# Kernel tuning notes

Measured on AMD Instinct MI355X. Metric: run time of the kernel, lower is better.

The kernel has to match this reference:

```python
import jax, jax.numpy as jnp
import numpy as np

B, LQ, LM, D, H = 2, 2048, 2048, 1024, 16
DH = D // H  # 64

def setup_inputs() -> dict:
    key = jax.random.key(0)
    ks = jax.random.split(key, 11)
    s = 0.02
    return {
        "query": jax.random.normal(ks[0], (B, LQ, D), jnp.float32),
        "memory": jax.random.normal(ks[1], (B, LM, D), jnp.float32),
        "memory_bias": jax.random.normal(ks[2], (B, LM), jnp.float32),
        "Wq": jax.random.normal(ks[3], (D, D), jnp.float32) * s,
        "bq": jnp.zeros((D,), jnp.float32),
        "Wk": jax.random.normal(ks[4], (D, D), jnp.float32) * s,
        "bk": jnp.zeros((D,), jnp.float32),
        "Wv": jax.random.normal(ks[5], (D, D), jnp.float32) * s,
        "bv": jnp.zeros((D,), jnp.float32),
        "Wo": jax.random.normal(ks[6], (D, D), jnp.float32) * s,
        "bo": jnp.zeros((D,), jnp.float32),
    }

def reference(query, memory, memory_bias, Wq, bq, Wk, bk, Wv, bv, Wo, bo):
    # QKV projections, split into heads: [B, L, H, DH]
    q = (query @ Wq + bq).reshape(B, LQ, H, DH)
    k = (memory @ Wk + bk).reshape(B, LM, H, DH)
    v = (memory @ Wv + bv).reshape(B, LM, H, DH)
    q = q * (DH ** -0.5)
    # logits: [B, H, Lq, Lk] (matches torch.einsum('btnh,bfnh->bnft', k, q))
    logits = jnp.einsum("bfnh,btnh->bnft", q, k)
    logits = logits + memory_bias[:, None, None, :]  # bias [B, Lm] -> [B,1,1,Lk]
    weights = jax.nn.softmax(logits, axis=-1)
    # dropout omitted (eval / rate 0 for correctness baseline)
    attn = jnp.einsum("bnft,btnh->bfnh", weights, v).reshape(B, LQ, D)
    return attn @ Wo + bo  # [B, Lq, output_depth]
```

## Files before the change

### kernel.cpp

```cpp
#include <hip/hip_runtime.h>
#include <hip/hip_bf16.h>
#include <math.h>


typedef __bf16 bf16;
typedef __bf16 bf16x4 __attribute__((ext_vector_type(4)));
typedef __bf16 bf16x8 __attribute__((ext_vector_type(8)));
typedef float f32x4 __attribute__((ext_vector_type(4)));

#define MFMA16(a, b, c) __builtin_amdgcn_mfma_f32_16x16x32_bf16((a), (b), (c), 0, 0, 0)

__device__ inline float exp2_hw(float x) {
    float r; asm("v_exp_f32 %0, %1" : "=v"(r) : "v"(x)); return r;
}

__device__ inline void gload_lds16(const bf16* g, bf16* l) {
    __builtin_amdgcn_global_load_lds(
        (const __attribute__((address_space(1))) void*)g,
        (__attribute__((address_space(3))) void*)l, 16, 0, 0);
}

__global__ __launch_bounds__(256) void prep_kernel(
    const float* __restrict__ query, const float* __restrict__ memory,
    const float* __restrict__ mbias,
    const float* __restrict__ W0, const float* __restrict__ W1,
    const float* __restrict__ W2, const float* __restrict__ W3,
    bf16* __restrict__ Yq, bf16* __restrict__ Ym, float* __restrict__ sbias,
    bf16* __restrict__ T0, bf16* __restrict__ T1,
    bf16* __restrict__ T2, bf16* __restrict__ T3)
{
    __shared__ float Ls[64][65];
    const int t = threadIdx.x;

    if (blockIdx.z == 0) {
        const float* X = blockIdx.y ? memory : query;
        bf16* Y = blockIdx.y ? Ym : Yq;
        const size_t i = ((size_t)blockIdx.x * 256 + t) * 8;
        float4 f0 = *(const float4*)&X[i];
        float4 f1 = *(const float4*)&X[i + 4];
        bf16x8 h;
        h[0] = (bf16)f0.x; h[1] = (bf16)f0.y; h[2] = (bf16)f0.z; h[3] = (bf16)f0.w;
        h[4] = (bf16)f1.x; h[5] = (bf16)f1.y; h[6] = (bf16)f1.z; h[7] = (bf16)f1.w;
        *(bf16x8*)&Y[i] = h;
        return;
    }
    const int x = blockIdx.x;
    if (x == 1024) {
        const int i = blockIdx.y * 2048 + t * 8;
        #pragma unroll
        for (int j = 0; j < 8; ++j) sbias[i + j] = mbias[i + j] * 1.44269504f;
        return;
    }
    if (x > 1024 || blockIdx.y) return;

    const int wsel = x >> 8, sub = x & 255;
    const float* W; bf16* T;
    switch (wsel) {
        case 0:  W = W0; T = T0; break;
        case 1:  W = W1; T = T1; break;
        case 2:  W = W2; T = T2; break;
        default: W = W3; T = T3; break;
    }
    const int n0 = (sub & 15) * 64, k0 = (sub >> 4) * 64;
    const int g = t >> 4, c = (t & 15) * 4;
    #pragma unroll
    for (int p = 0; p < 4; ++p) {
        const int row = p * 16 + g;
        float4 f = *(const float4*)&W[(size_t)(k0 + row) * 1024 + n0 + c];
        Ls[row][c + 0] = f.x; Ls[row][c + 1] = f.y;
        Ls[row][c + 2] = f.z; Ls[row][c + 3] = f.w;
    }
    __syncthreads();
    #pragma unroll
    for (int p = 0; p < 4; ++p) {
        const int n = p * 16 + g;
        bf16x4 h;
        h[0] = (bf16)Ls[c + 0][n]; h[1] = (bf16)Ls[c + 1][n];
        h[2] = (bf16)Ls[c + 2][n]; h[3] = (bf16)Ls[c + 3][n];
        *(bf16x4*)&T[(size_t)(n0 + n) * 1024 + k0 + c] = h;
    }
}

template <typename TO>
__global__ __launch_bounds__(256) void gemm_kernel(
    const bf16* __restrict__ A, const bf16* __restrict__ WT,
    const float* __restrict__ bias, TO* __restrict__ out,
    float alpha, int mode)
{
    __shared__ __align__(16) bf16 As[2][128 * 64];
    __shared__ __align__(16) bf16 Bs[2][64 * 64];

    const int fid = blockIdx.x + (blockIdx.y << 4);
    const int swz = (fid & 7) * 64 + (fid >> 3);
    const int n0 = (swz & 15) * 64;
    const int m0 = (swz >> 4) * 128;

    const int tid = threadIdx.x;
    const int w = tid >> 6, lane = tid & 63;
    const int lr = lane & 15, lg = lane >> 4;
    const int wm = (w >> 1) * 64, wn = (w & 1) * 32;

    const int arow0 = w * 32 + (lane >> 3);
    const int brow0 = w * 16 + (lane >> 3);
    const int sch = lane & 7;

    f32x4 acc[4][2] = {};

    auto stageG = [&](int kt, int bi) {
        #pragma unroll
        for (int p = 0; p < 4; ++p) {
            const int row = arow0 + p * 8;
            const int xc = ((sch ^ (row & 7)) << 3);
            gload_lds16(&A[(size_t)(m0 + row) * 1024 + kt + xc],
                        &As[bi][row * 64 + sch * 8]);
        }
        #pragma unroll
        for (int p = 0; p < 2; ++p) {
            const int row = brow0 + p * 8;
            const int xc = ((sch ^ (row & 7)) << 3);
            gload_lds16(&WT[(size_t)(n0 + row) * 1024 + kt + xc],
                        &Bs[bi][row * 64 + sch * 8]);
        }
    };

    stageG(0, 0);
    __syncthreads();

    int cur = 0;
    #pragma unroll 1
    for (int t = 0; t < 16; ++t) {
        if (t < 15) stageG((t + 1) * 64, cur ^ 1);

        #pragma unroll
        for (int ks = 0; ks < 2; ++ks) {
            const int c = (((ks * 4 + lg) ^ (lr & 7)) << 3);
            bf16x8 af[4], bfv[2];
            #pragma unroll
            for (int mt = 0; mt < 4; ++mt)
                af[mt] = *(const bf16x8*)&As[cur][(wm + mt * 16 + lr) * 64 + c];
            #pragma unroll
            for (int nt = 0; nt < 2; ++nt)
                bfv[nt] = *(const bf16x8*)&Bs[cur][(wn + nt * 16 + lr) * 64 + c];
            #pragma unroll
            for (int nt = 0; nt < 2; ++nt)
                #pragma unroll
                for (int mt = 0; mt < 4; ++mt)
                    acc[mt][nt] = MFMA16(af[mt], bfv[nt], acc[mt][nt]);
        }
        __syncthreads();
        cur ^= 1;
    }

    #pragma unroll
    for (int nt = 0; nt < 2; ++nt) {
        const int n = n0 + wn + nt * 16 + lr;
        const float bv = bias[n];
        #pragma unroll
        for (int mt = 0; mt < 4; ++mt) {
            #pragma unroll
            for (int i = 0; i < 4; ++i) {
                const int m = m0 + wm + mt * 16 + lg * 4 + i;
                const float v = (acc[mt][nt][i] + bv) * alpha;
                if (mode == 0) {
                    out[(size_t)m * 1024 + n] = (TO)v;
                } else {
                    const int b = m >> 11, t2 = m & 2047;
                    out[((size_t)(b << 10) + n) * 2048 + t2] = (TO)v;
                }
            }
        }
    }
}

__global__ __launch_bounds__(256) void gemm_kv_kernel(
    const bf16* __restrict__ A, const bf16* __restrict__ WTk,
    const bf16* __restrict__ WTv, const float* __restrict__ bk,
    const float* __restrict__ bv, bf16* __restrict__ Kout,
    bf16* __restrict__ Vtout)
{
    __shared__ __align__(16) bf16 As[2][128 * 64];
    __shared__ __align__(16) bf16 Bk[2][64 * 64];
    __shared__ __align__(16) bf16 Bv[2][64 * 64];

    const int fid = blockIdx.x + (blockIdx.y << 4);
    const int swz = (fid & 7) * 64 + (fid >> 3);
    const int n0 = (swz & 15) * 64;
    const int m0 = (swz >> 4) * 128;

    const int tid = threadIdx.x;
    const int w = tid >> 6, lane = tid & 63;
    const int lr = lane & 15, lg = lane >> 4;
    const int wm = (w >> 1) * 64, wn = (w & 1) * 32;

    const int arow0 = w * 32 + (lane >> 3);
    const int brow0 = w * 16 + (lane >> 3);
    const int sch = lane & 7;

    f32x4 accK[4][2] = {}, accV[4][2] = {};

    auto stageG = [&](int kt, int bi) {
        #pragma unroll
        for (int p = 0; p < 4; ++p) {
            const int row = arow0 + p * 8;
            const int xc = ((sch ^ (row & 7)) << 3);
            gload_lds16(&A[(size_t)(m0 + row) * 1024 + kt + xc],
                        &As[bi][row * 64 + sch * 8]);
        }
        #pragma unroll
        for (int p = 0; p < 2; ++p) {
            const int row = brow0 + p * 8;
            const int xc = ((sch ^ (row & 7)) << 3);
            gload_lds16(&WTk[(size_t)(n0 + row) * 1024 + kt + xc],
                        &Bk[bi][row * 64 + sch * 8]);
            gload_lds16(&WTv[(size_t)(n0 + row) * 1024 + kt + xc],
                        &Bv[bi][row * 64 + sch * 8]);
        }
    };

    stageG(0, 0);
    __syncthreads();

    int cur = 0;
    #pragma unroll 1
    for (int t = 0; t < 16; ++t) {
        if (t < 15) stageG((t + 1) * 64, cur ^ 1);

        #pragma unroll
        for (int ks = 0; ks < 2; ++ks) {
            const int c = (((ks * 4 + lg) ^ (lr & 7)) << 3);
            bf16x8 af[4], bkf[2], bvf[2];
            #pragma unroll
            for (int mt = 0; mt < 4; ++mt)
                af[mt] = *(const bf16x8*)&As[cur][(wm + mt * 16 + lr) * 64 + c];
            #pragma unroll
            for (int nt = 0; nt < 2; ++nt) {
                bkf[nt] = *(const bf16x8*)&Bk[cur][(wn + nt * 16 + lr) * 64 + c];
                bvf[nt] = *(const bf16x8*)&Bv[cur][(wn + nt * 16 + lr) * 64 + c];
            }
            #pragma unroll
            for (int nt = 0; nt < 2; ++nt)
                #pragma unroll
                for (int mt = 0; mt < 4; ++mt) {
                    accK[mt][nt] = MFMA16(af[mt], bkf[nt], accK[mt][nt]);
                    accV[mt][nt] = MFMA16(af[mt], bvf[nt], accV[mt][nt]);
                }
        }
        __syncthreads();
        cur ^= 1;
    }

    #pragma unroll
    for (int nt = 0; nt < 2; ++nt) {
        const int n = n0 + wn + nt * 16 + lr;
        const float bkv = bk[n], bvv = bv[n];
        #pragma unroll
        for (int mt = 0; mt < 4; ++mt) {
            #pragma unroll
            for (int i = 0; i < 4; ++i) {
                const int m = m0 + wm + mt * 16 + lg * 4 + i;
                Kout[(size_t)m * 1024 + n] = (bf16)(accK[mt][nt][i] + bkv);
                const int b = m >> 11, t2 = m & 2047;
                Vtout[((size_t)(b << 10) + n) * 2048 + t2] = (bf16)(accV[mt][nt][i] + bvv);
            }
        }
    }
}

__global__ __launch_bounds__(256) void attn_kernel(
    const bf16* __restrict__ Q, const bf16* __restrict__ K,
    const bf16* __restrict__ Vt, const float* __restrict__ sbias,
    bf16* __restrict__ Oout)
{
    __shared__ __align__(16) bf16 Kbuf[4][4096];
    __shared__ __align__(16) bf16 Vbuf[4][4096];

    const int tid = threadIdx.x;
    const int w = tid >> 6, lane = tid & 63;
    const int lr = lane & 15, lg = lane >> 4;

    const int fid = blockIdx.x + (blockIdx.y << 4) + (blockIdx.z << 8);
    const int swz = (fid & 7) * 64 + (fid >> 3);
    const int qt = swz & 15, head = (swz >> 4) & 15, b = swz >> 8;
    const int qrow = qt * 128 + w * 32;

    bf16x8 qf[2][2];
    #pragma unroll
    for (int g = 0; g < 2; ++g) {
        const size_t qo = (size_t)(b * 2048 + qrow + g * 16 + lr) * 1024 + head * 64;
        qf[g][0] = *(const bf16x8*)&Q[qo + lg * 8];
        qf[g][1] = *(const bf16x8*)&Q[qo + 32 + lg * 8];
    }

    const bf16* Kb = K + (size_t)b * 2048 * 1024 + head * 64;
    const bf16* Vb = Vt + ((size_t)b * 1024 + head * 64) * 2048;
    const float* biasb = sbias + b * 2048;

    float m_run[2] = {-INFINITY, -INFINITY};
    f32x4 of[2][4] = {};
    f32x4 ofl[2] = {};

    bf16x8 ones8;
    #pragma unroll
    for (int j = 0; j < 8; ++j) ones8[j] = (bf16)1.0f;

    auto stage = [&](int t, int slot) {
        #pragma unroll
        for (int cp = 0; cp < 2; ++cp) {
            const int chunk = cp * 256 + tid;
            const int R = chunk >> 3, cc = chunk & 7;
            const int cs = cc ^ (R & 7);
            const int piR = ((R & 16) << 1) | ((R & 12) << 1) | ((R & 32) >> 3) | (R & 3);
            gload_lds16(Kb + (size_t)(t * 64 + piR) * 1024 + cs * 8,
                        &Kbuf[slot][chunk * 8]);
            gload_lds16(Vb + (size_t)R * 2048 + t * 64 + cs * 8,
                        &Vbuf[slot][chunk * 8]);
        }
    };

    stage(0, 0);
    stage(1, 1);

    #pragma unroll 1
    for (int it = 0; it < 32; ++it) {
        const int slot = it & 3;
        const int tn = (it < 30) ? it + 2 : 31;
        stage(tn, (it + 2) & 3);
        asm volatile("s_waitcnt vmcnt(8)" ::: "memory");
        __builtin_amdgcn_s_barrier();
        __builtin_amdgcn_sched_barrier(0);

        const int bt = it * 64;
        f32x4 b4[4];
        b4[0] = *(const f32x4*)&biasb[bt + 8 * lg];
        b4[1] = *(const f32x4*)&biasb[bt + 32 + 8 * lg];
        b4[2] = *(const f32x4*)&biasb[bt + 4 + 8 * lg];
        b4[3] = *(const f32x4*)&biasb[bt + 36 + 8 * lg];

        f32x4 s[2][4];
        #pragma unroll
        for (int g = 0; g < 2; ++g)
            #pragma unroll
            for (int nt = 0; nt < 4; ++nt) s[g][nt] = b4[nt];
        #pragma unroll
        for (int ks = 0; ks < 2; ++ks) {
            const int cw = (((ks * 4 + lg) ^ (lr & 7)) << 3);
            bf16x8 kf[4];
            #pragma unroll
            for (int nt = 0; nt < 4; ++nt)
                kf[nt] = *(const bf16x8*)&Kbuf[slot][(nt * 16 + lr) * 64 + cw];
            __builtin_amdgcn_s_setprio(1);
            #pragma unroll
            for (int nt = 0; nt < 4; ++nt) {
                s[0][nt] = MFMA16(kf[nt], qf[0][ks], s[0][nt]);
                s[1][nt] = MFMA16(kf[nt], qf[1][ks], s[1][nt]);
            }
            __builtin_amdgcn_s_setprio(0);
        }

        float rml[2];
        #pragma unroll
        for (int g = 0; g < 2; ++g) {
            float m0 = fmaxf(fmaxf(s[g][0][0], s[g][0][1]), fmaxf(s[g][0][2], s[g][0][3]));
            float m1 = fmaxf(fmaxf(s[g][1][0], s[g][1][1]), fmaxf(s[g][1][2], s[g][1][3]));
            float m2 = fmaxf(fmaxf(s[g][2][0], s[g][2][1]), fmaxf(s[g][2][2], s[g][2][3]));
            float m3 = fmaxf(fmaxf(s[g][3][0], s[g][3][1]), fmaxf(s[g][3][2], s[g][3][3]));
            rml[g] = fmaxf(fmaxf(m0, m1), fmaxf(m2, m3));
        }
        const bool need = (rml[0] > m_run[0] + 8.f) || (rml[1] > m_run[1] + 8.f);

        if (__any(need)) {
            #pragma unroll
            for (int g = 0; g < 2; ++g) {
                float mx = fmaxf(rml[g], __shfl_xor(rml[g], 16, 64));
                mx = fmaxf(mx, __shfl_xor(mx, 32, 64));
                const float mnew = fmaxf(m_run[g], mx);
                const float al = exp2_hw(m_run[g] - mnew);
                m_run[g] = mnew;
                ofl[g] *= al;
                #pragma unroll
                for (int dt = 0; dt < 4; ++dt) of[g][dt] *= al;
            }
        }

        bf16x8 pb[2][2];
        #pragma unroll
        for (int g = 0; g < 2; ++g)
            #pragma unroll
            for (int i = 0; i < 4; ++i) {
                pb[g][0][i]     = (bf16)exp2_hw(s[g][0][i] - m_run[g]);
                pb[g][1][i]     = (bf16)exp2_hw(s[g][1][i] - m_run[g]);
                pb[g][0][4 + i] = (bf16)exp2_hw(s[g][2][i] - m_run[g]);
                pb[g][1][4 + i] = (bf16)exp2_hw(s[g][3][i] - m_run[g]);
            }

        __builtin_amdgcn_s_setprio(1);
        #pragma unroll
        for (int ks = 0; ks < 2; ++ks) {
            const int cw = (((ks * 4 + lg) ^ (lr & 7)) << 3);
            bf16x8 vf[4];
            #pragma unroll
            for (int dt = 0; dt < 4; ++dt)
                vf[dt] = *(const bf16x8*)&Vbuf[slot][(dt * 16 + lr) * 64 + cw];
            #pragma unroll
            for (int g = 0; g < 2; ++g) {
                #pragma unroll
                for (int dt = 0; dt < 4; ++dt)
                    of[g][dt] = MFMA16(vf[dt], pb[g][ks], of[g][dt]);
                ofl[g] = MFMA16(ones8, pb[g][ks], ofl[g]);
            }
        }
        __builtin_amdgcn_s_setprio(0);
    }

    #pragma unroll
    for (int g = 0; g < 2; ++g) {
        const float inv = 1.0f / ofl[g][0];
        const size_t ob = (size_t)(b * 2048 + qrow + g * 16 + lr) * 1024 + head * 64;
        #pragma unroll
        for (int dt = 0; dt < 4; ++dt) {
            bf16x4 h4;
            #pragma unroll
            for (int i = 0; i < 4; ++i) h4[i] = (bf16)(of[g][dt][i] * inv);
            *(bf16x4*)&Oout[ob + dt * 16 + lg * 4] = h4;
        }
    }
}

extern "C" void kernel_launch(void* const* d_in, const int* in_sizes, int n_in,
                              void* d_out, int out_size, void* d_ws, size_t ws_size,
                              hipStream_t stream) {
    const float* query  = (const float*)d_in[0];
    const float* memory = (const float*)d_in[1];
    const float* mbias  = (const float*)d_in[2];
    const float* Wq = (const float*)d_in[3];
    const float* bq = (const float*)d_in[4];
    const float* Wk = (const float*)d_in[5];
    const float* bk = (const float*)d_in[6];
    const float* Wv = (const float*)d_in[7];
    const float* bv = (const float*)d_in[8];
    const float* Wo = (const float*)d_in[9];
    const float* bo = (const float*)d_in[10];
    float* out = (float*)d_out;

    const size_t SZ = 4096ull * 1024ull * sizeof(bf16);
    const size_t WZ = 1024ull * 1024ull * sizeof(bf16);
    char* ws = (char*)d_ws;
    bf16* Qp  = (bf16*)(ws);
    bf16* Kp  = (bf16*)(ws + SZ);
    bf16* Vtp = (bf16*)(ws + 2 * SZ);
    bf16* Ap  = (bf16*)(ws + 3 * SZ);
    bf16* WTq = (bf16*)(ws + 4 * SZ);
    bf16* WTk = (bf16*)(ws + 4 * SZ + WZ);
    bf16* WTv = (bf16*)(ws + 4 * SZ + 2 * WZ);
    bf16* WTo = (bf16*)(ws + 4 * SZ + 3 * WZ);
    float* sbias = (float*)(ws + 4 * SZ + 4 * WZ);

    dim3 blk(256);
    prep_kernel<<<dim3(2048, 2, 2), blk, 0, stream>>>(
        query, memory, mbias, Wq, Wk, Wv, Wo, Kp, Ap, sbias, WTq, WTk, WTv, WTo);

    dim3 gg(16, 32);
    gemm_kernel<bf16><<<gg, blk, 0, stream>>>(Kp, WTq, bq, Qp, 0.18033688f, 0);
    gemm_kv_kernel<<<gg, blk, 0, stream>>>(Ap, WTk, WTv, bk, bv, Kp, Vtp);
    attn_kernel<<<dim3(16, 16, 2), blk, 0, stream>>>(Qp, Kp, Vtp, sbias, Ap);
    gemm_kernel<float><<<gg, blk, 0, stream>>>(Ap, WTo, bo, out, 1.0f, 0);
}
```

Measured before the change: 129.3 us.

## Use 512-thread attention blocks sharing K/V tiles, prefetch bias and V fragments

```diff
diff --git a/kernel.cpp b/kernel.cpp
--- a/kernel.cpp
+++ b/kernel.cpp
@@ -266,7 +266,7 @@
     }
 }
 
-__global__ __launch_bounds__(256) void attn_kernel(
+__global__ __launch_bounds__(512) void attn_kernel(
     const bf16* __restrict__ Q, const bf16* __restrict__ K,
     const bf16* __restrict__ Vt, const float* __restrict__ sbias,
     bf16* __restrict__ Oout)
@@ -278,10 +278,10 @@
     const int w = tid >> 6, lane = tid & 63;
     const int lr = lane & 15, lg = lane >> 4;
 
-    const int fid = blockIdx.x + (blockIdx.y << 4) + (blockIdx.z << 8);
-    const int swz = (fid & 7) * 64 + (fid >> 3);
-    const int qt = swz & 15, head = (swz >> 4) & 15, b = swz >> 8;
-    const int qrow = qt * 128 + w * 32;
+    const int fid = blockIdx.x + (blockIdx.y << 3) + (blockIdx.z << 7);
+    const int swz = (fid & 7) * 32 + (fid >> 3);
+    const int qt = swz & 7, head = (swz >> 3) & 15, b = swz >> 7;
+    const int qrow = qt * 256 + w * 32;
 
     bf16x8 qf[2][2];
     #pragma unroll
@@ -303,38 +303,40 @@
     #pragma unroll
     for (int j = 0; j < 8; ++j) ones8[j] = (bf16)1.0f;
 
+    const int R = tid >> 3, cc = tid & 7;
+    const int cs = cc ^ (R & 7);
+    const int piR = ((R & 16) << 1) | ((R & 12) << 1) | ((R & 32) >> 3) | (R & 3);
     auto stage = [&](int t, int slot) {
-        #pragma unroll
-        for (int cp = 0; cp < 2; ++cp) {
-            const int chunk = cp * 256 + tid;
-            const int R = chunk >> 3, cc = chunk & 7;
-            const int cs = cc ^ (R & 7);
-            const int piR = ((R & 16) << 1) | ((R & 12) << 1) | ((R & 32) >> 3) | (R & 3);
-            gload_lds16(Kb + (size_t)(t * 64 + piR) * 1024 + cs * 8,
-                        &Kbuf[slot][chunk * 8]);
-            gload_lds16(Vb + (size_t)R * 2048 + t * 64 + cs * 8,
-                        &Vbuf[slot][chunk * 8]);
-        }
+        gload_lds16(Kb + (size_t)(t * 64 + piR) * 1024 + cs * 8,
+                    &Kbuf[slot][tid * 8]);
+        gload_lds16(Vb + (size_t)R * 2048 + t * 64 + cs * 8,
+                    &Vbuf[slot][tid * 8]);
     };
 
     stage(0, 0);
     stage(1, 1);
+
+    f32x4 b4[4];
+    b4[0] = *(const f32x4*)&biasb[8 * lg];
+    b4[1] = *(const f32x4*)&biasb[32 + 8 * lg];
+    b4[2] = *(const f32x4*)&biasb[4 + 8 * lg];
+    b4[3] = *(const f32x4*)&biasb[36 + 8 * lg];
 
     #pragma unroll 1
     for (int it = 0; it < 32; ++it) {
         const int slot = it & 3;
         const int tn = (it < 30) ? it + 2 : 31;
         stage(tn, (it + 2) & 3);
-        asm volatile("s_waitcnt vmcnt(8)" ::: "memory");
+        asm volatile("s_waitcnt vmcnt(4)" ::: "memory");
         __builtin_amdgcn_s_barrier();
         __builtin_amdgcn_sched_barrier(0);
 
-        const int bt = it * 64;
-        f32x4 b4[4];
-        b4[0] = *(const f32x4*)&biasb[bt + 8 * lg];
-        b4[1] = *(const f32x4*)&biasb[bt + 32 + 8 * lg];
-        b4[2] = *(const f32x4*)&biasb[bt + 4 + 8 * lg];
-        b4[3] = *(const f32x4*)&biasb[bt + 36 + 8 * lg];
+        const int bt = ((it < 31) ? it + 1 : 31) * 64;
+        f32x4 b4n[4];
+        b4n[0] = *(const f32x4*)&biasb[bt + 8 * lg];
+        b4n[1] = *(const f32x4*)&biasb[bt + 32 + 8 * lg];
+        b4n[2] = *(const f32x4*)&biasb[bt + 4 + 8 * lg];
+        b4n[3] = *(const f32x4*)&biasb[bt + 36 + 8 * lg];
 
         f32x4 s[2][4];
         #pragma unroll
@@ -355,6 +357,15 @@
                 s[1][nt] = MFMA16(kf[nt], qf[1][ks], s[1][nt]);
             }
             __builtin_amdgcn_s_setprio(0);
+        }
+
+        bf16x8 vf[2][4];
+        #pragma unroll
+        for (int ks = 0; ks < 2; ++ks) {
+            const int cw = (((ks * 4 + lg) ^ (lr & 7)) << 3);
+            #pragma unroll
+            for (int dt = 0; dt < 4; ++dt)
+                vf[ks][dt] = *(const bf16x8*)&Vbuf[slot][(dt * 16 + lr) * 64 + cw];
         }
 
         float rml[2];
@@ -396,20 +407,18 @@
         __builtin_amdgcn_s_setprio(1);
         #pragma unroll
         for (int ks = 0; ks < 2; ++ks) {
-            const int cw = (((ks * 4 + lg) ^ (lr & 7)) << 3);
-            bf16x8 vf[4];
-            #pragma unroll
-            for (int dt = 0; dt < 4; ++dt)
-                vf[dt] = *(const bf16x8*)&Vbuf[slot][(dt * 16 + lr) * 64 + cw];
             #pragma unroll
             for (int g = 0; g < 2; ++g) {
                 #pragma unroll
                 for (int dt = 0; dt < 4; ++dt)
-                    of[g][dt] = MFMA16(vf[dt], pb[g][ks], of[g][dt]);
+                    of[g][dt] = MFMA16(vf[ks][dt], pb[g][ks], of[g][dt]);
                 ofl[g] = MFMA16(ones8, pb[g][ks], ofl[g]);
             }
         }
         __builtin_amdgcn_s_setprio(0);
+
+        #pragma unroll
+        for (int nt = 0; nt < 4; ++nt) b4[nt] = b4n[nt];
     }
 
     #pragma unroll
@@ -462,6 +471,6 @@
     dim3 gg(16, 32);
     gemm_kernel<bf16><<<gg, blk, 0, stream>>>(Kp, WTq, bq, Qp, 0.18033688f, 0);
     gemm_kv_kernel<<<gg, blk, 0, stream>>>(Ap, WTk, WTv, bk, bv, Kp, Vtp);
-    attn_kernel<<<dim3(16, 16, 2), blk, 0, stream>>>(Qp, Kp, Vtp, sbias, Ap);
+    attn_kernel<<<dim3(8, 16, 2), dim3(512), 0, stream>>>(Qp, Kp, Vtp, sbias, Ap);
     gemm_kernel<float><<<gg, blk, 0, stream>>>(Ap, WTo, bo, out, 1.0f, 0);
 }
```

Measured after the change: 120.7 us. 6.6% less time.
